# Performance work log

Measured on AMD Instinct MI355X. Metric: run time of the kernel, lower is better.

The kernel has to match this reference:

```python
import jax, jax.numpy as jnp
import numpy as np

N = 50000
E = 800000
EPS = 1e-5


def gcn_conv(x, W, b, src, dst, n):
    # PyG GCNConv: h = xW; add self-loops; symmetric norm D^-1/2 A_hat D^-1/2; out = agg + bias
    h = x @ W                                            # [N, out]
    deg = jax.ops.segment_sum(jnp.ones_like(src, dtype=h.dtype), dst, num_segments=n) + 1.0
    inv_sqrt = jax.lax.rsqrt(deg)                        # [N]
    coef = inv_sqrt[src] * inv_sqrt[dst]                 # [E]
    agg = jax.ops.segment_sum(h[src] * coef[:, None], dst, num_segments=n)
    agg = agg + h * (inv_sqrt * inv_sqrt)[:, None]       # self-loop term
    return agg + b


def batchnorm(h, gamma, beta):
    mean = jnp.mean(h, axis=0)
    var = jnp.var(h, axis=0)
    return gamma * (h - mean) * jax.lax.rsqrt(var + EPS) + beta


def setup_inputs() -> dict:
    key = jax.random.key(0)
    ks = jax.random.split(key, 8)
    x = jax.random.normal(ks[0], (N, 128), dtype=jnp.float32)
    edge_index = jax.random.randint(ks[1], (2, E), 0, N, dtype=jnp.int64)
    s = 1.0 / np.sqrt(128)
    W1 = jax.random.uniform(ks[2], (128, 128), jnp.float32, -s, s)
    W2 = jax.random.uniform(ks[3], (128, 128), jnp.float32, -s, s)
    W3 = jax.random.uniform(ks[4], (128, 64), jnp.float32, -s, s)
    b1 = jnp.zeros((128,), jnp.float32)
    b2 = jnp.zeros((128,), jnp.float32)
    b3 = jnp.zeros((64,), jnp.float32)
    g1 = jnp.ones((128,), jnp.float32)
    bt1 = jnp.zeros((128,), jnp.float32)
    g2 = jnp.ones((128,), jnp.float32)
    bt2 = jnp.zeros((128,), jnp.float32)
    return {"x": x, "edge_index": edge_index, "W1": W1, "b1": b1, "g1": g1, "bt1": bt1,
            "W2": W2, "b2": b2, "g2": g2, "bt2": bt2, "W3": W3, "b3": b3}


def reference(x, edge_index, W1, b1, g1, bt1, W2, b2, g2, bt2, W3, b3):
    src, dst = edge_index[0], edge_index[1]
    h = gcn_conv(x, W1, b1, src, dst, N)
    h = jax.nn.relu(batchnorm(h, g1, bt1))
    h = gcn_conv(h, W2, b2, src, dst, N)
    h = jax.nn.relu(batchnorm(h, g2, bt2))
    out = gcn_conv(h, W3, b3, src, dst, N)
    return out
```

## Files before the change

### kernel.cpp

```cpp
#include <hip/hip_runtime.h>

#define N_NODES 50000
#define N_EDGES 800000
static constexpr float EPS = 1e-5f;
static constexpr int SCAN_NB = (N_NODES + 255) / 256;
static constexpr int GEMM_NB = (N_NODES + 63) / 64;
static constexpr int FILL_NB = (N_EDGES + 1023) / 1024;

using bf16x8 = __attribute__((ext_vector_type(8))) short;
using f32x4  = __attribute__((ext_vector_type(4))) float;

static __device__ __forceinline__ unsigned short f2bf(float f) {
    unsigned int u = __float_as_uint(f);
    return (unsigned short)((u + 0x7FFFu + ((u >> 16) & 1u)) >> 16);
}
static __device__ __forceinline__ float blo(unsigned int w) { return __uint_as_float(w << 16); }
static __device__ __forceinline__ float bhi(unsigned int w) { return __uint_as_float(w & 0xffff0000u); }

__global__ __launch_bounds__(256) void k_prep_wconv(
    const int* __restrict__ ei, int* __restrict__ deg, int* __restrict__ rank,
    const float* __restrict__ W1, const float* __restrict__ W2,
    const float* __restrict__ W3,
    unsigned short* __restrict__ Wf1, unsigned short* __restrict__ Wf2,
    unsigned short* __restrict__ Wf3) {
    if (blockIdx.x < FILL_NB) {
        int e0 = (blockIdx.x * 256 + threadIdx.x) * 4;
        if (e0 >= N_EDGES) return;
        int4 d4 = *(const int4*)&ei[N_EDGES + e0];
        int4 r;
        r.x = atomicAdd(&deg[d4.x], 1);
        r.y = atomicAdd(&deg[d4.y], 1);
        r.z = atomicAdd(&deg[d4.z], 1);
        r.w = atomicAdd(&deg[d4.w], 1);
        *(int4*)&rank[e0] = r;
    } else {
        int gid = (blockIdx.x - FILL_NB) * 256 + threadIdx.x;
        const float* W; unsigned short* Wf; int NCOL, idx;
        if (gid < 16384)      { W = W1; Wf = Wf1; NCOL = 128; idx = gid; }
        else if (gid < 32768) { W = W2; Wf = Wf2; NCOL = 128; idx = gid - 16384; }
        else                  { W = W3; Wf = Wf3; NCOL = 64;  idx = gid - 32768; }
        int j  = idx & 7;
        int l  = (idx >> 3) & 63;
        int s  = (idx >> 9) & 3;
        int tn = idx >> 11;
        int n = tn * 16 + (l & 15);
        int k = s * 32 + (l >> 4) * 8 + j;
        Wf[idx] = f2bf(W[k * NCOL + n]);
    }
}

__global__ __launch_bounds__(256) void k_scan1(const int* __restrict__ deg,
                                               int* __restrict__ excl,
                                               int* __restrict__ partials) {
    const int t = threadIdx.x;
    const int i = blockIdx.x * 256 + t;
    int v = (i < N_NODES) ? deg[i] : 0;
    __shared__ int sh[256];
    sh[t] = v;
    __syncthreads();
    for (int off = 1; off < 256; off <<= 1) {
        int u = (t >= off) ? sh[t - off] : 0;
        __syncthreads();
        sh[t] += u;
        __syncthreads();
    }
    if (i < N_NODES) excl[i] = sh[t] - v;
    if (t == 255) partials[blockIdx.x] = sh[t];
}

__global__ __launch_bounds__(256) void k_scan23(const int* __restrict__ excl,
                                                const int* __restrict__ partials,
                                                const int* __restrict__ deg,
                                                int* __restrict__ rowptr,
                                                float* __restrict__ inv_sqrt) {
    const int t = threadIdx.x;
    int v = (t < SCAN_NB) ? partials[t] : 0;
    __shared__ int sh[256];
    __shared__ int base_s;
    sh[t] = v;
    __syncthreads();
    for (int off = 1; off < 256; off <<= 1) {
        int u = (t >= off) ? sh[t - off] : 0;
        __syncthreads();
        sh[t] += u;
        __syncthreads();
    }
    if (t == blockIdx.x) base_s = sh[t] - v;
    __syncthreads();
    const int base = base_s;
    const int i = blockIdx.x * 256 + t;
    if (i < N_NODES) {
        rowptr[i] = excl[i] + base;
        inv_sqrt[i] = rsqrtf((float)deg[i] + 1.0f);
    }
    if (i == 0) rowptr[N_NODES] = N_EDGES;
}

template <int NCOL, bool BN, bool ABF16>
static __device__ __forceinline__ void gemm_body(
    int row0, int t,
    const void* __restrict__ Ap, const unsigned short* __restrict__ Wf,
    const float* __restrict__ stats,
    const float* __restrict__ gamma, const float* __restrict__ beta,
    unsigned short* __restrict__ H,
    unsigned short* As, float* sc_s, float* sh_s) {
    if (BN) {
        if (t < 128) {
            float s  = stats[t];
            float sq = stats[128 + t];
            float mean = s * (1.0f / N_NODES);
            float var  = sq * (1.0f / N_NODES) - mean * mean;
            float sc = gamma[t] * rsqrtf(var + EPS);
            sc_s[t] = sc;
            sh_s[t] = beta[t] - mean * sc;
        }
        __syncthreads();
    }

#pragma unroll
    for (int i = 0; i < 4; i++) {
        int q = i * 256 + t;
        int row = q >> 4;
        int c8  = (q & 15) * 8;
        int grow = row0 + row;
        float v[8];
        if (grow < N_NODES) {
            if (ABF16) {
                uint4 p = *(const uint4*)((const unsigned short*)Ap + (size_t)grow * 128 + c8);
                v[0] = blo(p.x); v[1] = bhi(p.x); v[2] = blo(p.y); v[3] = bhi(p.y);
                v[4] = blo(p.z); v[5] = bhi(p.z); v[6] = blo(p.w); v[7] = bhi(p.w);
            } else {
                const float* Af = (const float*)Ap + (size_t)grow * 128 + c8;
                float4 f0 = *(const float4*)Af;
                float4 f1 = *(const float4*)(Af + 4);
                v[0] = f0.x; v[1] = f0.y; v[2] = f0.z; v[3] = f0.w;
                v[4] = f1.x; v[5] = f1.y; v[6] = f1.z; v[7] = f1.w;
            }
        } else {
#pragma unroll
            for (int j = 0; j < 8; j++) v[j] = 0.f;
        }
        if (BN) {
#pragma unroll
            for (int j = 0; j < 8; j++)
                v[j] = fmaxf(fmaf(v[j], sc_s[c8 + j], sh_s[c8 + j]), 0.f);
        }
        uint4 pk;
        pk.x = (unsigned)f2bf(v[0]) | ((unsigned)f2bf(v[1]) << 16);
        pk.y = (unsigned)f2bf(v[2]) | ((unsigned)f2bf(v[3]) << 16);
        pk.z = (unsigned)f2bf(v[4]) | ((unsigned)f2bf(v[5]) << 16);
        pk.w = (unsigned)f2bf(v[6]) | ((unsigned)f2bf(v[7]) << 16);
        *(uint4*)&As[row * 136 + c8] = pk;
    }
    __syncthreads();

    const int wv = t >> 6;
    const int l  = t & 63;
    const int m  = l & 15;
    const int kq = l >> 4;

    bf16x8 afrag[4];
    const unsigned short* arow = &As[(wv * 16 + m) * 136 + kq * 8];
#pragma unroll
    for (int s = 0; s < 4; s++)
        afrag[s] = *(const bf16x8*)(arow + s * 32);

    constexpr int NT = NCOL / 16;
#pragma unroll
    for (int tn = 0; tn < NT; tn++) {
        f32x4 acc = {0.f, 0.f, 0.f, 0.f};
#pragma unroll
        for (int s = 0; s < 4; s++) {
            bf16x8 b = *(const bf16x8*)&Wf[(size_t)((tn * 4 + s) * 64 + l) * 8];
            acc = __builtin_amdgcn_mfma_f32_16x16x32_bf16(afrag[s], b, acc, 0, 0, 0);
        }
        int col = tn * 16 + m;
#pragma unroll
        for (int r = 0; r < 4; r++) {
            int row = row0 + wv * 16 + kq * 4 + r;
            if (row < N_NODES) H[(size_t)row * NCOL + col] = f2bf(acc[r]);
        }
    }
}

template <int NCOL>
__global__ __launch_bounds__(256) void k_gemm_bn(
    const unsigned short* __restrict__ A, const unsigned short* __restrict__ Wf,
    const float* __restrict__ stats,
    const float* __restrict__ gamma, const float* __restrict__ beta,
    unsigned short* __restrict__ H) {
    __shared__ unsigned short As[64 * 136];
    __shared__ float sc_s[128], sh_s[128];
    gemm_body<NCOL, true, true>(blockIdx.x * 64, threadIdx.x, A, Wf, stats,
                                gamma, beta, H, As, sc_s, sh_s);
}

__global__ __launch_bounds__(256) void k_gemm1_fill(
    const float* __restrict__ x, const unsigned short* __restrict__ Wf1,
    unsigned short* __restrict__ h1,
    const int* __restrict__ ei, const int* __restrict__ rank,
    const int* __restrict__ rowptr, int* __restrict__ esrc) {
    __shared__ unsigned short As[64 * 136];
    __shared__ float sc_s[128], sh_s[128];
    if (blockIdx.x < GEMM_NB) {
        gemm_body<128, false, false>(blockIdx.x * 64, threadIdx.x, x, Wf1,
                                     nullptr, nullptr, nullptr, h1, As, sc_s, sh_s);
    } else {
        int e0 = ((blockIdx.x - GEMM_NB) * 256 + threadIdx.x) * 4;
        if (e0 < N_EDGES) {
            int4 s4 = *(const int4*)&ei[e0];
            int4 d4 = *(const int4*)&ei[N_EDGES + e0];
            int4 r4 = *(const int4*)&rank[e0];
            int p0 = rowptr[d4.x] + r4.x;
            int p1 = rowptr[d4.y] + r4.y;
            int p2 = rowptr[d4.z] + r4.z;
            int p3 = rowptr[d4.w] + r4.w;
            esrc[p0] = s4.x;
            esrc[p1] = s4.y;
            esrc[p2] = s4.z;
            esrc[p3] = s4.w;
        }
    }
}

template <int F, bool OUTBF>
__global__ __launch_bounds__(256) void k_agg(const int* __restrict__ rowptr,
                                             const int* __restrict__ esrc,
                                             const float* __restrict__ inv_sqrt,
                                             const unsigned short* __restrict__ H,
                                             const float* __restrict__ bias,
                                             void* __restrict__ OUT) {
    constexpr int LPN = F / 8;
    constexpr int NPB = 256 / LPN;
    const int t = threadIdx.x;
    const int node = blockIdx.x * NPB + t / LPN;
    const int lane = t % LPN;
    if (node >= N_NODES) return;

    const uint4* __restrict__ Hv = (const uint4*)H;
    const int beg = rowptr[node];
    const int end = rowptr[node + 1];
    const float rsn = inv_sqrt[node];

    float acc[8];
#pragma unroll
    for (int i = 0; i < 8; i++) acc[i] = 0.f;

#define ACC8(P, C)                                                     \
    acc[0] = fmaf(blo((P).x), (C), acc[0]);                            \
    acc[1] = fmaf(bhi((P).x), (C), acc[1]);                            \
    acc[2] = fmaf(blo((P).y), (C), acc[2]);                            \
    acc[3] = fmaf(bhi((P).y), (C), acc[3]);                            \
    acc[4] = fmaf(blo((P).z), (C), acc[4]);                            \
    acc[5] = fmaf(bhi((P).z), (C), acc[5]);                            \
    acc[6] = fmaf(blo((P).w), (C), acc[6]);                            \
    acc[7] = fmaf(bhi((P).w), (C), acc[7]);

    int j = beg;
    for (; j + 3 < end; j += 4) {
        int s0 = esrc[j], s1 = esrc[j + 1], s2 = esrc[j + 2], s3 = esrc[j + 3];
        uint4 p0 = Hv[(size_t)s0 * LPN + lane];
        uint4 p1 = Hv[(size_t)s1 * LPN + lane];
        uint4 p2 = Hv[(size_t)s2 * LPN + lane];
        uint4 p3 = Hv[(size_t)s3 * LPN + lane];
        float c0 = inv_sqrt[s0] * rsn, c1 = inv_sqrt[s1] * rsn;
        float c2 = inv_sqrt[s2] * rsn, c3 = inv_sqrt[s3] * rsn;
        ACC8(p0, c0) ACC8(p1, c1) ACC8(p2, c2) ACC8(p3, c3)
    }
    for (; j < end; j++) {
        int s0 = esrc[j];
        float c0 = inv_sqrt[s0] * rsn;
        uint4 p0 = Hv[(size_t)s0 * LPN + lane];
        ACC8(p0, c0)
    }
#undef ACC8

    uint4 ps = Hv[(size_t)node * LPN + lane];
    float idv = rsn * rsn;
    float4 b0 = ((const float4*)bias)[lane * 2];
    float4 b1 = ((const float4*)bias)[lane * 2 + 1];
    acc[0] = fmaf(blo(ps.x), idv, acc[0]) + b0.x;
    acc[1] = fmaf(bhi(ps.x), idv, acc[1]) + b0.y;
    acc[2] = fmaf(blo(ps.y), idv, acc[2]) + b0.z;
    acc[3] = fmaf(bhi(ps.y), idv, acc[3]) + b0.w;
    acc[4] = fmaf(blo(ps.z), idv, acc[4]) + b1.x;
    acc[5] = fmaf(bhi(ps.z), idv, acc[5]) + b1.y;
    acc[6] = fmaf(blo(ps.w), idv, acc[6]) + b1.z;
    acc[7] = fmaf(bhi(ps.w), idv, acc[7]) + b1.w;

    if (OUTBF) {
        uint4 pk;
        pk.x = (unsigned)f2bf(acc[0]) | ((unsigned)f2bf(acc[1]) << 16);
        pk.y = (unsigned)f2bf(acc[2]) | ((unsigned)f2bf(acc[3]) << 16);
        pk.z = (unsigned)f2bf(acc[4]) | ((unsigned)f2bf(acc[5]) << 16);
        pk.w = (unsigned)f2bf(acc[6]) | ((unsigned)f2bf(acc[7]) << 16);
        ((uint4*)OUT)[(size_t)node * LPN + lane] = pk;
    } else {
        float4* o = (float4*)OUT + ((size_t)node * LPN + lane) * 2;
        o[0] = make_float4(acc[0], acc[1], acc[2], acc[3]);
        o[1] = make_float4(acc[4], acc[5], acc[6], acc[7]);
    }
}

__global__ __launch_bounds__(256) void k_stats(const unsigned short* __restrict__ A,
                                               float* __restrict__ stats) {
    const int t  = threadIdx.x;
    const int c4 = t & 31;
    const int rr = t >> 5;
    float4 sum = make_float4(0.f, 0.f, 0.f, 0.f);
    float4 sq  = make_float4(0.f, 0.f, 0.f, 0.f);
    for (int row = blockIdx.x * 8 + rr; row < N_NODES; row += gridDim.x * 8) {
        uint2 p = *(const uint2*)&A[(size_t)row * 128 + c4 * 4];
        float vx = blo(p.x), vy = bhi(p.x), vz = blo(p.y), vw = bhi(p.y);
        sum.x += vx; sum.y += vy; sum.z += vz; sum.w += vw;
        sq.x += vx * vx; sq.y += vy * vy; sq.z += vz * vz; sq.w += vw * vw;
    }
    __shared__ float4 red[2][8][32];
    red[0][rr][c4] = sum;
    red[1][rr][c4] = sq;
    __syncthreads();
    if (t < 32) {
        float4 s = make_float4(0.f, 0.f, 0.f, 0.f);
        float4 q = make_float4(0.f, 0.f, 0.f, 0.f);
#pragma unroll
        for (int i = 0; i < 8; i++) {
            float4 a = red[0][i][t];
            float4 b = red[1][i][t];
            s.x += a.x; s.y += a.y; s.z += a.z; s.w += a.w;
            q.x += b.x; q.y += b.y; q.z += b.z; q.w += b.w;
        }
        int c = t * 4;
        atomicAdd(&stats[c + 0], s.x); atomicAdd(&stats[c + 1], s.y);
        atomicAdd(&stats[c + 2], s.z); atomicAdd(&stats[c + 3], s.w);
        atomicAdd(&stats[128 + c + 0], q.x); atomicAdd(&stats[128 + c + 1], q.y);
        atomicAdd(&stats[128 + c + 2], q.z); atomicAdd(&stats[128 + c + 3], q.w);
    }
}

extern "C" void kernel_launch(void* const* d_in, const int* in_sizes, int n_in,
                              void* d_out, int out_size, void* d_ws, size_t ws_size,
                              hipStream_t stream) {
    const float* x   = (const float*)d_in[0];
    const int*   ei  = (const int*)d_in[1];
    const float* W1  = (const float*)d_in[2];
    const float* b1  = (const float*)d_in[3];
    const float* g1  = (const float*)d_in[4];
    const float* bt1 = (const float*)d_in[5];
    const float* W2  = (const float*)d_in[6];
    const float* b2  = (const float*)d_in[7];
    const float* g2  = (const float*)d_in[8];
    const float* bt2 = (const float*)d_in[9];
    const float* W3  = (const float*)d_in[10];
    const float* b3  = (const float*)d_in[11];
    float* out = (float*)d_out;

    char* ws = (char*)d_ws;
    size_t off = 0;
    auto alloc = [&](size_t bytes) { char* p = ws + off; off += (bytes + 255) & ~(size_t)255; return p; };
    int*   deg      = (int*)  alloc((size_t)N_NODES * 4);
    float* stats1   = (float*)alloc(256 * 4);
    float* stats2   = (float*)alloc(256 * 4);
    const size_t zbytes = (size_t)((char*)(stats2 + 256) - (char*)deg);
    float* inv_sqrt = (float*)alloc((size_t)N_NODES * 4);
    int*   excl     = (int*)  alloc((size_t)N_NODES * 4);
    int*   partials = (int*)  alloc(256 * 4);
    int*   rowptr   = (int*)  alloc((size_t)(N_NODES + 1) * 4);
    int*   rank     = (int*)  alloc((size_t)N_EDGES * 4);
    int*   esrc     = (int*)  alloc((size_t)N_EDGES * 4);
    unsigned short* Wf1 = (unsigned short*)alloc((size_t)128 * 128 * 2);
    unsigned short* Wf2 = (unsigned short*)alloc((size_t)128 * 128 * 2);
    unsigned short* Wf3 = (unsigned short*)alloc((size_t)64 * 128 * 2);
    unsigned short* h1  = (unsigned short*)alloc((size_t)N_NODES * 128 * 2);
    unsigned short* h2  = (unsigned short*)alloc((size_t)N_NODES * 128 * 2);
    unsigned short* h3  = (unsigned short*)alloc((size_t)N_NODES * 64 * 2);
    unsigned short* agg1 = (unsigned short*)alloc((size_t)N_NODES * 128 * 2);
    unsigned short* agg2 = (unsigned short*)alloc((size_t)N_NODES * 128 * 2);

    hipMemsetAsync(deg, 0, zbytes, stream);

    k_prep_wconv<<<FILL_NB + 160, 256, 0, stream>>>(ei, deg, rank, W1, W2, W3,
                                                    Wf1, Wf2, Wf3);
    k_scan1<<<SCAN_NB, 256, 0, stream>>>(deg, excl, partials);
    k_scan23<<<SCAN_NB, 256, 0, stream>>>(excl, partials, deg, rowptr, inv_sqrt);

    k_gemm1_fill<<<GEMM_NB + FILL_NB, 256, 0, stream>>>(x, Wf1, h1, ei, rank, rowptr, esrc);

    k_agg<128, true><<<N_NODES / 16, 256, 0, stream>>>(rowptr, esrc, inv_sqrt, h1, b1, agg1);
    k_stats<<<256, 256, 0, stream>>>(agg1, stats1);

    k_gemm_bn<128><<<GEMM_NB, 256, 0, stream>>>(agg1, Wf2, stats1, g1, bt1, h2);
    k_agg<128, true><<<N_NODES / 16, 256, 0, stream>>>(rowptr, esrc, inv_sqrt, h2, b2, agg2);
    k_stats<<<256, 256, 0, stream>>>(agg2, stats2);

    k_gemm_bn<64><<<GEMM_NB, 256, 0, stream>>>(agg2, Wf3, stats2, g2, bt2, h3);
    k_agg<64, false><<<(N_NODES + 31) / 32, 256, 0, stream>>>(rowptr, esrc, inv_sqrt, h3, b3, out);
}
```

Before: 320.6 us.

## Split degree counting into per-chunk arrays and overlap it with first GEMM

Degree atomics now go to 7 separate per-chunk count arrays, which is meant to spread contention on shared counters. The atomic degree pass is fused into the same launch as the first GEMM so the two run concurrently. The weight conversion runs in its own launch beforehand. The scan combines the chunk counts into per-chunk offsets, and the CSR fill becomes a separate kernel. This adds one kernel launch, a larger memset, and extra memory traffic for the chunked counts.

New measurement: 315.7 us. About the same (-1.5%).

```diff
diff --git a/kernel.cpp b/kernel.cpp
--- a/kernel.cpp
+++ b/kernel.cpp
@@ -3,6 +3,8 @@
 #define N_NODES 50000
 #define N_EDGES 800000
 static constexpr float EPS = 1e-5f;
+static constexpr int NP = 50048;
+static constexpr int NCHUNK = 7;
 static constexpr int SCAN_NB = (N_NODES + 255) / 256;
 static constexpr int GEMM_NB = (N_NODES + 63) / 64;
 static constexpr int FILL_NB = (N_EDGES + 1023) / 1024;
@@ -17,83 +19,23 @@
 static __device__ __forceinline__ float blo(unsigned int w) { return __uint_as_float(w << 16); }
 static __device__ __forceinline__ float bhi(unsigned int w) { return __uint_as_float(w & 0xffff0000u); }
 
-__global__ __launch_bounds__(256) void k_prep_wconv(
-    const int* __restrict__ ei, int* __restrict__ deg, int* __restrict__ rank,
+__global__ __launch_bounds__(256) void k_wconv_all(
     const float* __restrict__ W1, const float* __restrict__ W2,
     const float* __restrict__ W3,
     unsigned short* __restrict__ Wf1, unsigned short* __restrict__ Wf2,
     unsigned short* __restrict__ Wf3) {
-    if (blockIdx.x < FILL_NB) {
-        int e0 = (blockIdx.x * 256 + threadIdx.x) * 4;
-        if (e0 >= N_EDGES) return;
-        int4 d4 = *(const int4*)&ei[N_EDGES + e0];
-        int4 r;
-        r.x = atomicAdd(&deg[d4.x], 1);
-        r.y = atomicAdd(&deg[d4.y], 1);
-        r.z = atomicAdd(&deg[d4.z], 1);
-        r.w = atomicAdd(&deg[d4.w], 1);
-        *(int4*)&rank[e0] = r;
-    } else {
-        int gid = (blockIdx.x - FILL_NB) * 256 + threadIdx.x;
-        const float* W; unsigned short* Wf; int NCOL, idx;
-        if (gid < 16384)      { W = W1; Wf = Wf1; NCOL = 128; idx = gid; }
-        else if (gid < 32768) { W = W2; Wf = Wf2; NCOL = 128; idx = gid - 16384; }
-        else                  { W = W3; Wf = Wf3; NCOL = 64;  idx = gid - 32768; }
-        int j  = idx & 7;
-        int l  = (idx >> 3) & 63;
-        int s  = (idx >> 9) & 3;
-        int tn = idx >> 11;
-        int n = tn * 16 + (l & 15);
-        int k = s * 32 + (l >> 4) * 8 + j;
-        Wf[idx] = f2bf(W[k * NCOL + n]);
-    }
-}
-
-__global__ __launch_bounds__(256) void k_scan1(const int* __restrict__ deg,
-                                               int* __restrict__ excl,
-                                               int* __restrict__ partials) {
-    const int t = threadIdx.x;
-    const int i = blockIdx.x * 256 + t;
-    int v = (i < N_NODES) ? deg[i] : 0;
-    __shared__ int sh[256];
-    sh[t] = v;
-    __syncthreads();
-    for (int off = 1; off < 256; off <<= 1) {
-        int u = (t >= off) ? sh[t - off] : 0;
-        __syncthreads();
-        sh[t] += u;
-        __syncthreads();
-    }
-    if (i < N_NODES) excl[i] = sh[t] - v;
-    if (t == 255) partials[blockIdx.x] = sh[t];
-}
-
-__global__ __launch_bounds__(256) void k_scan23(const int* __restrict__ excl,
-                                                const int* __restrict__ partials,
-                                                const int* __restrict__ deg,
-                                                int* __restrict__ rowptr,
-                                                float* __restrict__ inv_sqrt) {
-    const int t = threadIdx.x;
-    int v = (t < SCAN_NB) ? partials[t] : 0;
-    __shared__ int sh[256];
-    __shared__ int base_s;
-    sh[t] = v;
-    __syncthreads();
-    for (int off = 1; off < 256; off <<= 1) {
-        int u = (t >= off) ? sh[t - off] : 0;
-        __syncthreads();
-        sh[t] += u;
-        __syncthreads();
-    }
-    if (t == blockIdx.x) base_s = sh[t] - v;
-    __syncthreads();
-    const int base = base_s;
-    const int i = blockIdx.x * 256 + t;
-    if (i < N_NODES) {
-        rowptr[i] = excl[i] + base;
-        inv_sqrt[i] = rsqrtf((float)deg[i] + 1.0f);
-    }
-    if (i == 0) rowptr[N_NODES] = N_EDGES;
+    int gid = blockIdx.x * 256 + threadIdx.x;
+    const float* W; unsigned short* Wf; int NCOL, idx;
+    if (gid < 16384)      { W = W1; Wf = Wf1; NCOL = 128; idx = gid; }
+    else if (gid < 32768) { W = W2; Wf = Wf2; NCOL = 128; idx = gid - 16384; }
+    else                  { W = W3; Wf = Wf3; NCOL = 64;  idx = gid - 32768; }
+    int j  = idx & 7;
+    int l  = (idx >> 3) & 63;
+    int s  = (idx >> 9) & 3;
+    int tn = idx >> 11;
+    int n = tn * 16 + (l & 15);
+    int k = s * 32 + (l >> 4) * 8 + j;
+    Wf[idx] = f2bf(W[k * NCOL + n]);
 }
 
 template <int NCOL, bool BN, bool ABF16>
@@ -195,32 +137,110 @@
                                 gamma, beta, H, As, sc_s, sh_s);
 }
 
-__global__ __launch_bounds__(256) void k_gemm1_fill(
+__global__ __launch_bounds__(256) void k_prep_gemm1(
+    const int* __restrict__ ei, int* __restrict__ deg8, int* __restrict__ rank,
     const float* __restrict__ x, const unsigned short* __restrict__ Wf1,
-    unsigned short* __restrict__ h1,
-    const int* __restrict__ ei, const int* __restrict__ rank,
-    const int* __restrict__ rowptr, int* __restrict__ esrc) {
+    unsigned short* __restrict__ h1) {
     __shared__ unsigned short As[64 * 136];
     __shared__ float sc_s[128], sh_s[128];
-    if (blockIdx.x < GEMM_NB) {
-        gemm_body<128, false, false>(blockIdx.x * 64, threadIdx.x, x, Wf1,
-                                     nullptr, nullptr, nullptr, h1, As, sc_s, sh_s);
+    if (blockIdx.x < FILL_NB) {
+        int e0 = (blockIdx.x * 256 + threadIdx.x) * 4;
+        if (e0 >= N_EDGES) return;
+        int* dchunk = deg8 + (e0 >> 17) * NP;
+        int4 d4 = *(const int4*)&ei[N_EDGES + e0];
+        int4 r;
+        r.x = atomicAdd(&dchunk[d4.x], 1);
+        r.y = atomicAdd(&dchunk[d4.y], 1);
+        r.z = atomicAdd(&dchunk[d4.z], 1);
+        r.w = atomicAdd(&dchunk[d4.w], 1);
+        *(int4*)&rank[e0] = r;
     } else {
-        int e0 = ((blockIdx.x - GEMM_NB) * 256 + threadIdx.x) * 4;
-        if (e0 < N_EDGES) {
-            int4 s4 = *(const int4*)&ei[e0];
-            int4 d4 = *(const int4*)&ei[N_EDGES + e0];
-            int4 r4 = *(const int4*)&rank[e0];
-            int p0 = rowptr[d4.x] + r4.x;
-            int p1 = rowptr[d4.y] + r4.y;
-            int p2 = rowptr[d4.z] + r4.z;
-            int p3 = rowptr[d4.w] + r4.w;
-            esrc[p0] = s4.x;
-            esrc[p1] = s4.y;
-            esrc[p2] = s4.z;
-            esrc[p3] = s4.w;
-        }
-    }
+        gemm_body<128, false, false>((blockIdx.x - FILL_NB) * 64, threadIdx.x,
+                                     x, Wf1, nullptr, nullptr, nullptr, h1,
+                                     As, sc_s, sh_s);
+    }
+}
+
+__global__ __launch_bounds__(256) void k_scan1(int* __restrict__ deg8,
+                                               float* __restrict__ inv_sqrt,
+                                               int* __restrict__ excl,
+                                               int* __restrict__ partials) {
+    const int t = threadIdx.x;
+    const int i = blockIdx.x * 256 + t;
+    int tot = 0;
+    if (i < N_NODES) {
+        int cb[NCHUNK];
+        int run = 0;
+#pragma unroll
+        for (int c = 0; c < NCHUNK; c++) {
+            int v = deg8[c * NP + i];
+            cb[c] = run;
+            run += v;
+        }
+        tot = run;
+#pragma unroll
+        for (int c = 0; c < NCHUNK; c++) deg8[c * NP + i] = cb[c];
+        inv_sqrt[i] = rsqrtf((float)tot + 1.0f);
+    }
+    __shared__ int sh[256];
+    sh[t] = tot;
+    __syncthreads();
+    for (int off = 1; off < 256; off <<= 1) {
+        int u = (t >= off) ? sh[t - off] : 0;
+        __syncthreads();
+        sh[t] += u;
+        __syncthreads();
+    }
+    if (i < N_NODES) excl[i] = sh[t] - tot;
+    if (t == 255) partials[blockIdx.x] = sh[t];
+}
+
+__global__ __launch_bounds__(256) void k_scan23(const int* __restrict__ excl,
+                                                const int* __restrict__ partials,
+                                                int* __restrict__ rowptr,
+                                                int* __restrict__ deg8) {
+    const int t = threadIdx.x;
+    int v = (t < SCAN_NB) ? partials[t] : 0;
+    __shared__ int sh[256];
+    __shared__ int base_s;
+    sh[t] = v;
+    __syncthreads();
+    for (int off = 1; off < 256; off <<= 1) {
+        int u = (t >= off) ? sh[t - off] : 0;
+        __syncthreads();
+        sh[t] += u;
+        __syncthreads();
+    }
+    if (t == blockIdx.x) base_s = sh[t] - v;
+    __syncthreads();
+    const int i = blockIdx.x * 256 + t;
+    if (i < N_NODES) {
+        int r = excl[i] + base_s;
+        rowptr[i] = r;
+#pragma unroll
+        for (int c = 0; c < NCHUNK; c++) deg8[c * NP + i] += r;
+    }
+    if (i == 0) rowptr[N_NODES] = N_EDGES;
+}
+
+__global__ __launch_bounds__(256) void k_fill(const int* __restrict__ ei,
+                                              const int* __restrict__ rank,
+                                              const int* __restrict__ deg8,
+                                              int* __restrict__ esrc) {
+    int e0 = (blockIdx.x * 256 + threadIdx.x) * 4;
+    if (e0 >= N_EDGES) return;
+    const int* sb = deg8 + (e0 >> 17) * NP;
+    int4 s4 = *(const int4*)&ei[e0];
+    int4 d4 = *(const int4*)&ei[N_EDGES + e0];
+    int4 r4 = *(const int4*)&rank[e0];
+    int p0 = sb[d4.x] + r4.x;
+    int p1 = sb[d4.y] + r4.y;
+    int p2 = sb[d4.z] + r4.z;
+    int p3 = sb[d4.w] + r4.w;
+    esrc[p0] = s4.x;
+    esrc[p1] = s4.y;
+    esrc[p2] = s4.z;
+    esrc[p3] = s4.w;
 }
 
 template <int F, bool OUTBF>
@@ -357,10 +377,10 @@
     char* ws = (char*)d_ws;
     size_t off = 0;
     auto alloc = [&](size_t bytes) { char* p = ws + off; off += (bytes + 255) & ~(size_t)255; return p; };
-    int*   deg      = (int*)  alloc((size_t)N_NODES * 4);
+    int*   deg8     = (int*)  alloc((size_t)NCHUNK * NP * 4);
     float* stats1   = (float*)alloc(256 * 4);
     float* stats2   = (float*)alloc(256 * 4);
-    const size_t zbytes = (size_t)((char*)(stats2 + 256) - (char*)deg);
+    const size_t zbytes = (size_t)((char*)(stats2 + 256) - (char*)deg8);
     float* inv_sqrt = (float*)alloc((size_t)N_NODES * 4);
     int*   excl     = (int*)  alloc((size_t)N_NODES * 4);
     int*   partials = (int*)  alloc(256 * 4);
@@ -376,14 +396,15 @@
     unsigned short* agg1 = (unsigned short*)alloc((size_t)N_NODES * 128 * 2);
     unsigned short* agg2 = (unsigned short*)alloc((size_t)N_NODES * 128 * 2);
 
-    hipMemsetAsync(deg, 0, zbytes, stream);
-
-    k_prep_wconv<<<FILL_NB + 160, 256, 0, stream>>>(ei, deg, rank, W1, W2, W3,
-                                                    Wf1, Wf2, Wf3);
-    k_scan1<<<SCAN_NB, 256, 0, stream>>>(deg, excl, partials);
-    k_scan23<<<SCAN_NB, 256, 0, stream>>>(excl, partials, deg, rowptr, inv_sqrt);
-
-    k_gemm1_fill<<<GEMM_NB + FILL_NB, 256, 0, stream>>>(x, Wf1, h1, ei, rank, rowptr, esrc);
+    hipMemsetAsync(deg8, 0, zbytes, stream);
+
+    k_wconv_all<<<160, 256, 0, stream>>>(W1, W2, W3, Wf1, Wf2, Wf3);
+
+    k_prep_gemm1<<<FILL_NB + GEMM_NB, 256, 0, stream>>>(ei, deg8, rank, x, Wf1, h1);
+
+    k_scan1<<<SCAN_NB, 256, 0, stream>>>(deg8, inv_sqrt, excl, partials);
+    k_scan23<<<SCAN_NB, 256, 0, stream>>>(excl, partials, rowptr, deg8);
+    k_fill<<<FILL_NB, 256, 0, stream>>>(ei, rank, deg8, esrc);
 
     k_agg<128, true><<<N_NODES / 16, 256, 0, stream>>>(rowptr, esrc, inv_sqrt, h1, b1, agg1);
     k_stats<<<256, 256, 0, stream>>>(agg1, stats1);
```

## Fuse all GCN stages into one persistent cooperative kernel with grid syncs

Applied to the files above, without the earlier changes.

Replaces the sequence of about ten separate kernel launches and the memset with a single cooperative persistent kernel. Blocks loop over work items for each stage and a grid-wide barrier separates dependent stages. This removes launch gaps and per-kernel tail effects. In exchange it adds grid barrier costs and caps occupancy at one shared-memory configuration for all stages, which may be worse for the memory-bound aggregation phases. It also hardcodes 256 CUs when sizing the grid.

Result: slower. 946.5 us (+195.2%).

```diff
diff --git a/kernel.cpp b/kernel.cpp
--- a/kernel.cpp
+++ b/kernel.cpp
@@ -1,11 +1,18 @@
 #include <hip/hip_runtime.h>
+#include <hip/hip_cooperative_groups.h>
+
+namespace cg = cooperative_groups;
 
 #define N_NODES 50000
 #define N_EDGES 800000
 static constexpr float EPS = 1e-5f;
-static constexpr int SCAN_NB = (N_NODES + 255) / 256;
-static constexpr int GEMM_NB = (N_NODES + 63) / 64;
-static constexpr int FILL_NB = (N_EDGES + 1023) / 1024;
+static constexpr int SCAN_NB  = (N_NODES + 255) / 256;
+static constexpr int GEMM_NB  = (N_NODES + 63) / 64;
+static constexpr int FILL_NB  = (N_EDGES + 1023) / 1024;
+static constexpr int AGG128_NB = N_NODES / 16;
+static constexpr int AGG64_NB  = (N_NODES + 31) / 32;
+static constexpr int STATS_NB  = 256;
+static constexpr int WCONV_N   = 40960;
 
 using bf16x8 = __attribute__((ext_vector_type(8))) short;
 using f32x4  = __attribute__((ext_vector_type(4))) float;
@@ -17,84 +24,21 @@
 static __device__ __forceinline__ float blo(unsigned int w) { return __uint_as_float(w << 16); }
 static __device__ __forceinline__ float bhi(unsigned int w) { return __uint_as_float(w & 0xffff0000u); }
 
-__global__ __launch_bounds__(256) void k_prep_wconv(
-    const int* __restrict__ ei, int* __restrict__ deg, int* __restrict__ rank,
-    const float* __restrict__ W1, const float* __restrict__ W2,
-    const float* __restrict__ W3,
-    unsigned short* __restrict__ Wf1, unsigned short* __restrict__ Wf2,
-    unsigned short* __restrict__ Wf3) {
-    if (blockIdx.x < FILL_NB) {
-        int e0 = (blockIdx.x * 256 + threadIdx.x) * 4;
-        if (e0 >= N_EDGES) return;
-        int4 d4 = *(const int4*)&ei[N_EDGES + e0];
-        int4 r;
-        r.x = atomicAdd(&deg[d4.x], 1);
-        r.y = atomicAdd(&deg[d4.y], 1);
-        r.z = atomicAdd(&deg[d4.z], 1);
-        r.w = atomicAdd(&deg[d4.w], 1);
-        *(int4*)&rank[e0] = r;
-    } else {
-        int gid = (blockIdx.x - FILL_NB) * 256 + threadIdx.x;
-        const float* W; unsigned short* Wf; int NCOL, idx;
-        if (gid < 16384)      { W = W1; Wf = Wf1; NCOL = 128; idx = gid; }
-        else if (gid < 32768) { W = W2; Wf = Wf2; NCOL = 128; idx = gid - 16384; }
-        else                  { W = W3; Wf = Wf3; NCOL = 64;  idx = gid - 32768; }
-        int j  = idx & 7;
-        int l  = (idx >> 3) & 63;
-        int s  = (idx >> 9) & 3;
-        int tn = idx >> 11;
-        int n = tn * 16 + (l & 15);
-        int k = s * 32 + (l >> 4) * 8 + j;
-        Wf[idx] = f2bf(W[k * NCOL + n]);
-    }
-}
-
-__global__ __launch_bounds__(256) void k_scan1(const int* __restrict__ deg,
-                                               int* __restrict__ excl,
-                                               int* __restrict__ partials) {
-    const int t = threadIdx.x;
-    const int i = blockIdx.x * 256 + t;
-    int v = (i < N_NODES) ? deg[i] : 0;
-    __shared__ int sh[256];
-    sh[t] = v;
-    __syncthreads();
-    for (int off = 1; off < 256; off <<= 1) {
-        int u = (t >= off) ? sh[t - off] : 0;
-        __syncthreads();
-        sh[t] += u;
-        __syncthreads();
-    }
-    if (i < N_NODES) excl[i] = sh[t] - v;
-    if (t == 255) partials[blockIdx.x] = sh[t];
-}
-
-__global__ __launch_bounds__(256) void k_scan23(const int* __restrict__ excl,
-                                                const int* __restrict__ partials,
-                                                const int* __restrict__ deg,
-                                                int* __restrict__ rowptr,
-                                                float* __restrict__ inv_sqrt) {
-    const int t = threadIdx.x;
-    int v = (t < SCAN_NB) ? partials[t] : 0;
-    __shared__ int sh[256];
-    __shared__ int base_s;
-    sh[t] = v;
-    __syncthreads();
-    for (int off = 1; off < 256; off <<= 1) {
-        int u = (t >= off) ? sh[t - off] : 0;
-        __syncthreads();
-        sh[t] += u;
-        __syncthreads();
-    }
-    if (t == blockIdx.x) base_s = sh[t] - v;
-    __syncthreads();
-    const int base = base_s;
-    const int i = blockIdx.x * 256 + t;
-    if (i < N_NODES) {
-        rowptr[i] = excl[i] + base;
-        inv_sqrt[i] = rsqrtf((float)deg[i] + 1.0f);
-    }
-    if (i == 0) rowptr[N_NODES] = N_EDGES;
-}
+struct MegaParams {
+    const int* ei;
+    const float* x;
+    const float* W1; const float* W2; const float* W3;
+    const float* b1; const float* g1; const float* bt1;
+    const float* b2; const float* g2; const float* bt2;
+    const float* b3;
+    float* out;
+    int* deg; int* excl; int* partials; int* rowptr; int* rank; int* esrc;
+    float* inv_sqrt; float* stats1; float* stats2;
+    unsigned short* Wf1; unsigned short* Wf2; unsigned short* Wf3;
+    unsigned short* h1; unsigned short* h2; unsigned short* h3;
+    unsigned short* agg1; unsigned short* agg2;
+    int zero16;
+};
 
 template <int NCOL, bool BN, bool ABF16>
 static __device__ __forceinline__ void gemm_body(
@@ -181,59 +125,17 @@
             if (row < N_NODES) H[(size_t)row * NCOL + col] = f2bf(acc[r]);
         }
     }
-}
-
-template <int NCOL>
-__global__ __launch_bounds__(256) void k_gemm_bn(
-    const unsigned short* __restrict__ A, const unsigned short* __restrict__ Wf,
-    const float* __restrict__ stats,
-    const float* __restrict__ gamma, const float* __restrict__ beta,
-    unsigned short* __restrict__ H) {
-    __shared__ unsigned short As[64 * 136];
-    __shared__ float sc_s[128], sh_s[128];
-    gemm_body<NCOL, true, true>(blockIdx.x * 64, threadIdx.x, A, Wf, stats,
-                                gamma, beta, H, As, sc_s, sh_s);
-}
-
-__global__ __launch_bounds__(256) void k_gemm1_fill(
-    const float* __restrict__ x, const unsigned short* __restrict__ Wf1,
-    unsigned short* __restrict__ h1,
-    const int* __restrict__ ei, const int* __restrict__ rank,
-    const int* __restrict__ rowptr, int* __restrict__ esrc) {
-    __shared__ unsigned short As[64 * 136];
-    __shared__ float sc_s[128], sh_s[128];
-    if (blockIdx.x < GEMM_NB) {
-        gemm_body<128, false, false>(blockIdx.x * 64, threadIdx.x, x, Wf1,
-                                     nullptr, nullptr, nullptr, h1, As, sc_s, sh_s);
-    } else {
-        int e0 = ((blockIdx.x - GEMM_NB) * 256 + threadIdx.x) * 4;
-        if (e0 < N_EDGES) {
-            int4 s4 = *(const int4*)&ei[e0];
-            int4 d4 = *(const int4*)&ei[N_EDGES + e0];
-            int4 r4 = *(const int4*)&rank[e0];
-            int p0 = rowptr[d4.x] + r4.x;
-            int p1 = rowptr[d4.y] + r4.y;
-            int p2 = rowptr[d4.z] + r4.z;
-            int p3 = rowptr[d4.w] + r4.w;
-            esrc[p0] = s4.x;
-            esrc[p1] = s4.y;
-            esrc[p2] = s4.z;
-            esrc[p3] = s4.w;
-        }
-    }
+    __syncthreads();
 }
 
 template <int F, bool OUTBF>
-__global__ __launch_bounds__(256) void k_agg(const int* __restrict__ rowptr,
-                                             const int* __restrict__ esrc,
-                                             const float* __restrict__ inv_sqrt,
-                                             const unsigned short* __restrict__ H,
-                                             const float* __restrict__ bias,
-                                             void* __restrict__ OUT) {
+static __device__ __forceinline__ void agg_item(
+    int w, int t, const int* __restrict__ rowptr, const int* __restrict__ esrc,
+    const float* __restrict__ inv_sqrt, const unsigned short* __restrict__ H,
+    const float* __restrict__ bias, void* __restrict__ OUT) {
     constexpr int LPN = F / 8;
     constexpr int NPB = 256 / LPN;
-    const int t = threadIdx.x;
-    const int node = blockIdx.x * NPB + t / LPN;
+    const int node = w * NPB + t / LPN;
     const int lane = t % LPN;
     if (node >= N_NODES) return;
 
@@ -302,20 +204,19 @@
     }
 }
 
-__global__ __launch_bounds__(256) void k_stats(const unsigned short* __restrict__ A,
-                                               float* __restrict__ stats) {
-    const int t  = threadIdx.x;
+static __device__ __forceinline__ void stats_item(
+    int w, int t, const unsigned short* __restrict__ A, float* __restrict__ stats,
+    float4 (*red)[8][32]) {
     const int c4 = t & 31;
     const int rr = t >> 5;
     float4 sum = make_float4(0.f, 0.f, 0.f, 0.f);
     float4 sq  = make_float4(0.f, 0.f, 0.f, 0.f);
-    for (int row = blockIdx.x * 8 + rr; row < N_NODES; row += gridDim.x * 8) {
+    for (int row = w * 8 + rr; row < N_NODES; row += STATS_NB * 8) {
         uint2 p = *(const uint2*)&A[(size_t)row * 128 + c4 * 4];
         float vx = blo(p.x), vy = bhi(p.x), vz = blo(p.y), vw = bhi(p.y);
         sum.x += vx; sum.y += vy; sum.z += vz; sum.w += vw;
         sq.x += vx * vx; sq.y += vy * vy; sq.z += vz * vz; sq.w += vw * vw;
     }
-    __shared__ float4 red[2][8][32];
     red[0][rr][c4] = sum;
     red[1][rr][c4] = sq;
     __syncthreads();
@@ -335,63 +236,188 @@
         atomicAdd(&stats[128 + c + 0], q.x); atomicAdd(&stats[128 + c + 1], q.y);
         atomicAdd(&stats[128 + c + 2], q.z); atomicAdd(&stats[128 + c + 3], q.w);
     }
+    __syncthreads();
+}
+
+__global__ __launch_bounds__(256, 4) void k_mega(MegaParams p) {
+    cg::grid_group grid = cg::this_grid();
+    const int t   = threadIdx.x;
+    const int bid = blockIdx.x;
+    const int nb  = gridDim.x;
+    const int gtid = bid * 256 + t;
+    const int gsz  = nb * 256;
+
+    __shared__ unsigned short As[64 * 136];
+    __shared__ float sc_s[128], sh_s[128];
+    __shared__ int shi[256];
+    __shared__ float4 red[2][8][32];
+
+    {
+        int4* z = (int4*)p.deg;
+        for (int i = gtid; i < p.zero16; i += gsz) z[i] = make_int4(0, 0, 0, 0);
+        for (int gid = gtid; gid < WCONV_N; gid += gsz) {
+            const float* W; unsigned short* Wf; int NCOL, idx;
+            if (gid < 16384)      { W = p.W1; Wf = p.Wf1; NCOL = 128; idx = gid; }
+            else if (gid < 32768) { W = p.W2; Wf = p.Wf2; NCOL = 128; idx = gid - 16384; }
+            else                  { W = p.W3; Wf = p.Wf3; NCOL = 64;  idx = gid - 32768; }
+            int j  = idx & 7;
+            int l  = (idx >> 3) & 63;
+            int s  = (idx >> 9) & 3;
+            int tn = idx >> 11;
+            int n = tn * 16 + (l & 15);
+            int k = s * 32 + (l >> 4) * 8 + j;
+            Wf[idx] = f2bf(W[k * NCOL + n]);
+        }
+    }
+    grid.sync();
+
+    for (int w = bid; w < FILL_NB + GEMM_NB; w += nb) {
+        if (w < FILL_NB) {
+            int e0 = (w * 256 + t) * 4;
+            if (e0 < N_EDGES) {
+                int4 d4 = *(const int4*)&p.ei[N_EDGES + e0];
+                int4 r;
+                r.x = atomicAdd(&p.deg[d4.x], 1);
+                r.y = atomicAdd(&p.deg[d4.y], 1);
+                r.z = atomicAdd(&p.deg[d4.z], 1);
+                r.w = atomicAdd(&p.deg[d4.w], 1);
+                *(int4*)&p.rank[e0] = r;
+            }
+        } else {
+            gemm_body<128, false, false>((w - FILL_NB) * 64, t, p.x, p.Wf1,
+                                         nullptr, nullptr, nullptr, p.h1,
+                                         As, sc_s, sh_s);
+        }
+    }
+    grid.sync();
+
+    for (int w = bid; w < SCAN_NB; w += nb) {
+        int i = w * 256 + t;
+        int v = (i < N_NODES) ? p.deg[i] : 0;
+        if (i < N_NODES) p.inv_sqrt[i] = rsqrtf((float)v + 1.0f);
+        shi[t] = v;
+        __syncthreads();
+        for (int off = 1; off < 256; off <<= 1) {
+            int u = (t >= off) ? shi[t - off] : 0;
+            __syncthreads();
+            shi[t] += u;
+            __syncthreads();
+        }
+        if (i < N_NODES) p.excl[i] = shi[t] - v;
+        if (t == 255) p.partials[w] = shi[t];
+        __syncthreads();
+    }
+    grid.sync();
+
+    for (int w = bid; w < SCAN_NB; w += nb) {
+        int v = (t < SCAN_NB) ? p.partials[t] : 0;
+        shi[t] = v;
+        __syncthreads();
+        for (int off = 1; off < 256; off <<= 1) {
+            int u = (t >= off) ? shi[t - off] : 0;
+            __syncthreads();
+            shi[t] += u;
+            __syncthreads();
+        }
+        int base = shi[w] - p.partials[w];
+        int i = w * 256 + t;
+        if (i < N_NODES) p.rowptr[i] = p.excl[i] + base;
+        if (i == 0) p.rowptr[N_NODES] = N_EDGES;
+        __syncthreads();
+    }
+    grid.sync();
+
+    for (int w = bid; w < FILL_NB; w += nb) {
+        int e0 = (w * 256 + t) * 4;
+        if (e0 < N_EDGES) {
+            int4 s4 = *(const int4*)&p.ei[e0];
+            int4 d4 = *(const int4*)&p.ei[N_EDGES + e0];
+            int4 r4 = *(const int4*)&p.rank[e0];
+            p.esrc[p.rowptr[d4.x] + r4.x] = s4.x;
+            p.esrc[p.rowptr[d4.y] + r4.y] = s4.y;
+            p.esrc[p.rowptr[d4.z] + r4.z] = s4.z;
+            p.esrc[p.rowptr[d4.w] + r4.w] = s4.w;
+        }
+    }
+    grid.sync();
+
+    for (int w = bid; w < AGG128_NB; w += nb)
+        agg_item<128, true>(w, t, p.rowptr, p.esrc, p.inv_sqrt, p.h1, p.b1, p.agg1);
+    grid.sync();
+
+    for (int w = bid; w < STATS_NB; w += nb)
+        stats_item(w, t, p.agg1, p.stats1, red);
+    grid.sync();
+
+    for (int w = bid; w < GEMM_NB; w += nb)
+        gemm_body<128, true, true>(w * 64, t, p.agg1, p.Wf2, p.stats1,
+                                   p.g1, p.bt1, p.h2, As, sc_s, sh_s);
+    grid.sync();
+
+    for (int w = bid; w < AGG128_NB; w += nb)
+        agg_item<128, true>(w, t, p.rowptr, p.esrc, p.inv_sqrt, p.h2, p.b2, p.agg2);
+    grid.sync();
+
+    for (int w = bid; w < STATS_NB; w += nb)
+        stats_item(w, t, p.agg2, p.stats2, red);
+    grid.sync();
+
+    for (int w = bid; w < GEMM_NB; w += nb)
+        gemm_body<64, true, true>(w * 64, t, p.agg2, p.Wf3, p.stats2,
+                                  p.g2, p.bt2, p.h3, As, sc_s, sh_s);
+    grid.sync();
+
+    for (int w = bid; w < AGG64_NB; w += nb)
+        agg_item<64, false>(w, t, p.rowptr, p.esrc, p.inv_sqrt, p.h3, p.b3, p.out);
 }
 
 extern "C" void kernel_launch(void* const* d_in, const int* in_sizes, int n_in,
                               void* d_out, int out_size, void* d_ws, size_t ws_size,
                               hipStream_t stream) {
-    const float* x   = (const float*)d_in[0];
-    const int*   ei  = (const int*)d_in[1];
-    const float* W1  = (const float*)d_in[2];
-    const float* b1  = (const float*)d_in[3];
-    const float* g1  = (const float*)d_in[4];
-    const float* bt1 = (const float*)d_in[5];
-    const float* W2  = (const float*)d_in[6];
-    const float* b2  = (const float*)d_in[7];
-    const float* g2  = (const float*)d_in[8];
-    const float* bt2 = (const float*)d_in[9];
-    const float* W3  = (const float*)d_in[10];
-    const float* b3  = (const float*)d_in[11];
-    float* out = (float*)d_out;
+    MegaParams p;
+    p.ei  = (const int*)d_in[1];
+    p.x   = (const float*)d_in[0];
+    p.W1  = (const float*)d_in[2];
+    p.b1  = (const float*)d_in[3];
+    p.g1  = (const float*)d_in[4];
+    p.bt1 = (const float*)d_in[5];
+    p.W2  = (const float*)d_in[6];
+    p.b2  = (const float*)d_in[7];
+    p.g2  = (const float*)d_in[8];
+    p.bt2 = (const float*)d_in[9];
+    p.W3  = (const float*)d_in[10];
+    p.b3  = (const float*)d_in[11];
+    p.out = (float*)d_out;
 
     char* ws = (char*)d_ws;
     size_t off = 0;
-    auto alloc = [&](size_t bytes) { char* p = ws + off; off += (bytes + 255) & ~(size_t)255; return p; };
-    int*   deg      = (int*)  alloc((size_t)N_NODES * 4);
-    float* stats1   = (float*)alloc(256 * 4);
-    float* stats2   = (float*)alloc(256 * 4);
-    const size_t zbytes = (size_t)((char*)(stats2 + 256) - (char*)deg);
-    float* inv_sqrt = (float*)alloc((size_t)N_NODES * 4);
-    int*   excl     = (int*)  alloc((size_t)N_NODES * 4);
-    int*   partials = (int*)  alloc(256 * 4);
-    int*   rowptr   = (int*)  alloc((size_t)(N_NODES + 1) * 4);
-    int*   rank     = (int*)  alloc((size_t)N_EDGES * 4);
-    int*   esrc     = (int*)  alloc((size_t)N_EDGES * 4);
-    unsigned short* Wf1 = (unsigned short*)alloc((size_t)128 * 128 * 2);
-    unsigned short* Wf2 = (unsigned short*)alloc((size_t)128 * 128 * 2);
-    unsigned short* Wf3 = (unsigned short*)alloc((size_t)64 * 128 * 2);
-    unsigned short* h1  = (unsigned short*)alloc((size_t)N_NODES * 128 * 2);
-    unsigned short* h2  = (unsigned short*)alloc((size_t)N_NODES * 128 * 2);
-    unsigned short* h3  = (unsigned short*)alloc((size_t)N_NODES * 64 * 2);
-    unsigned short* agg1 = (unsigned short*)alloc((size_t)N_NODES * 128 * 2);
-    unsigned short* agg2 = (unsigned short*)alloc((size_t)N_NODES * 128 * 2);
-
-    hipMemsetAsync(deg, 0, zbytes, stream);
-
-    k_prep_wconv<<<FILL_NB + 160, 256, 0, stream>>>(ei, deg, rank, W1, W2, W3,
-                                                    Wf1, Wf2, Wf3);
-    k_scan1<<<SCAN_NB, 256, 0, stream>>>(deg, excl, partials);
-    k_scan23<<<SCAN_NB, 256, 0, stream>>>(excl, partials, deg, rowptr, inv_sqrt);
-
-    k_gemm1_fill<<<GEMM_NB + FILL_NB, 256, 0, stream>>>(x, Wf1, h1, ei, rank, rowptr, esrc);
-
-    k_agg<128, true><<<N_NODES / 16, 256, 0, stream>>>(rowptr, esrc, inv_sqrt, h1, b1, agg1);
-    k_stats<<<256, 256, 0, stream>>>(agg1, stats1);
-
-    k_gemm_bn<128><<<GEMM_NB, 256, 0, stream>>>(agg1, Wf2, stats1, g1, bt1, h2);
-    k_agg<128, true><<<N_NODES / 16, 256, 0, stream>>>(rowptr, esrc, inv_sqrt, h2, b2, agg2);
-    k_stats<<<256, 256, 0, stream>>>(agg2, stats2);
-
-    k_gemm_bn<64><<<GEMM_NB, 256, 0, stream>>>(agg2, Wf3, stats2, g2, bt2, h3);
-    k_agg<64, false><<<(N_NODES + 31) / 32, 256, 0, stream>>>(rowptr, esrc, inv_sqrt, h3, b3, out);
-}
+    auto alloc = [&](size_t bytes) { char* q = ws + off; off += (bytes + 255) & ~(size_t)255; return q; };
+    p.deg     = (int*)  alloc((size_t)N_NODES * 4);
+    p.stats1  = (float*)alloc(256 * 4);
+    p.stats2  = (float*)alloc(256 * 4);
+    const size_t zbytes = (size_t)((char*)(p.stats2 + 256) - (char*)p.deg);
+    p.zero16  = (int)(zbytes / 16);
+    p.inv_sqrt = (float*)alloc((size_t)N_NODES * 4);
+    p.excl     = (int*)  alloc((size_t)N_NODES * 4);
+    p.partials = (int*)  alloc(256 * 4);
+    p.rowptr   = (int*)  alloc((size_t)(N_NODES + 1) * 4);
+    p.rank     = (int*)  alloc((size_t)N_EDGES * 4);
+    p.esrc     = (int*)  alloc((size_t)N_EDGES * 4);
+    p.Wf1 = (unsigned short*)alloc((size_t)128 * 128 * 2);
+    p.Wf2 = (unsigned short*)alloc((size_t)128 * 128 * 2);
+    p.Wf3 = (unsigned short*)alloc((size_t)64 * 128 * 2);
+    p.h1  = (unsigned short*)alloc((size_t)N_NODES * 128 * 2);
+    p.h2  = (unsigned short*)alloc((size_t)N_NODES * 128 * 2);
+    p.h3  = (unsigned short*)alloc((size_t)N_NODES * 64 * 2);
+    p.agg1 = (unsigned short*)alloc((size_t)N_NODES * 128 * 2);
+    p.agg2 = (unsigned short*)alloc((size_t)N_NODES * 128 * 2);
+
+    int maxB = 0;
+    hipOccupancyMaxActiveBlocksPerMultiprocessor(&maxB, k_mega, 256, 0);
+    if (maxB < 1) maxB = 1;
+    int grid = maxB * 256;
+    if (grid > 2048) grid = 2048;
+
+    void* args[] = { &p };
+    hipLaunchCooperativeKernel((void*)k_mega, dim3(grid), dim3(256), args, 0, stream);
+}
```
